# Kernel optimization log

Hardware: AMD Instinct MI355X
Metric: run time of the kernel (lower is better)

## Reference

```python
import jax, jax.numpy as jnp
import numpy as np

N_NODES = 100000
N_EDGES = 3200000
IN_DIM = 128
H1, F1 = 8, 8          # layer1: 8 heads x 8 feats -> concat 64
N_CLASSES = 40         # layer2: 1 head -> classes
NEG_SLOPE = 0.2        # GAT LeakyReLU slope


def setup_inputs() -> dict:
    key = jax.random.key(0)
    ks = jax.random.split(key, 8)
    x = jax.random.normal(ks[0], (N_NODES, IN_DIM), dtype=jnp.float32)
    adj = jax.random.randint(ks[1], (2, N_EDGES), 0, N_NODES, dtype=jnp.int64)
    s1 = 1.0 / np.sqrt(IN_DIM)
    s2 = 1.0 / np.sqrt(H1 * F1)
    W1 = jax.random.normal(ks[2], (IN_DIM, H1 * F1), dtype=jnp.float32) * s1
    a1_src = jax.random.normal(ks[3], (H1, F1), dtype=jnp.float32) * s2
    a1_dst = jax.random.normal(ks[4], (H1, F1), dtype=jnp.float32) * s2
    W2 = jax.random.normal(ks[5], (H1 * F1, N_CLASSES), dtype=jnp.float32) * s2
    a2_src = jax.random.normal(ks[6], (1, N_CLASSES), dtype=jnp.float32) * s2
    a2_dst = jax.random.normal(ks[7], (1, N_CLASSES), dtype=jnp.float32) * s2
    return {"input_matrix": x, "adjacency_coo_matrix": adj,
            "W1": W1, "a1_src": a1_src, "a1_dst": a1_dst,
            "W2": W2, "a2_src": a2_src, "a2_dst": a2_dst}


def gat_layer(x, src, dst, W, a_s, a_d, heads, fdim):
    n = x.shape[0]
    h = (x @ W).reshape(n, heads, fdim)                 # [N,H,F]
    e_src = jnp.sum(h * a_s, axis=-1)                   # [N,H]
    e_dst = jnp.sum(h * a_d, axis=-1)                   # [N,H]
    e = jax.nn.leaky_relu(e_src[src] + e_dst[dst], NEG_SLOPE)  # [E,H]
    m = jax.ops.segment_max(e, dst, num_segments=n)     # per-dst softmax max
    p = jnp.exp(e - m[dst])
    s = jax.ops.segment_sum(p, dst, num_segments=n)
    alpha = p / s[dst]                                  # [E,H]
    out = jax.ops.segment_sum(alpha[:, :, None] * h[src], dst, num_segments=n)
    return out                                          # [N,H,F]


def reference(input_matrix, adjacency_coo_matrix, W1, a1_src, a1_dst, W2, a2_src, a2_dst):
    n = input_matrix.shape[0]
    loops = jnp.arange(n, dtype=adjacency_coo_matrix.dtype)
    src = jnp.concatenate([adjacency_coo_matrix[0], loops])
    dst = jnp.concatenate([adjacency_coo_matrix[1], loops])
    x = gat_layer(input_matrix, src, dst, W1, a1_src, a1_dst, H1, F1)
    x = jax.nn.elu(x.reshape(n, H1 * F1))               # concat heads + ELU
    x = gat_layer(x, src, dst, W2, a2_src, a2_dst, 1, N_CLASSES)
    return jax.nn.log_softmax(x.reshape(n, N_CLASSES), axis=1)
```

## Files before the change

### kernel.cpp

```cpp
#include <hip/hip_runtime.h>
#include <hip/hip_fp16.h>
#include <math.h>

#define NN 100000
#define EE 3200000
#define ET (EE + NN)
#define BKW 128
#define NBK ((NN + BKW - 1) / BKW)
#define BCAP 5120
#define EPB 4096
#define NB_P1 ((EE + EPB - 1) / EPB)
#define NB_G 391

typedef float v2f __attribute__((ext_vector_type(2)));
typedef float v4f __attribute__((ext_vector_type(4)));
typedef _Float16 v8h __attribute__((ext_vector_type(8)));

__device__ __forceinline__ float lrelu(float v) { return fmaxf(v, 0.2f * v); }

__device__ __forceinline__ unsigned char to_fp8(float v) {
  return (unsigned char)(__builtin_amdgcn_cvt_pk_fp8_f32(v, v, 0, false) & 0xff);
}


__global__ __launch_bounds__(256) void k_p1(const int* __restrict__ srcs,
                                            const int* __restrict__ dsts,
                                            int* __restrict__ bcount,
                                            int* __restrict__ bbuf) {
  __shared__ int lcnt[NBK];
  __shared__ int lbase[NBK];
  int tid = threadIdx.x;
  for (int i = tid; i < NBK; i += 256) lcnt[i] = 0;
  __syncthreads();
  int e0 = blockIdx.x * EPB;
  int rank[16], bkt[16], pk[16];
#pragma unroll
  for (int i = 0; i < 16; ++i) {
    int e = e0 + tid + i * 256;
    bkt[i] = -1;
    if (e < EE) {
      int d = dsts[e];
      int s = srcs[e];
      int b = d >> 7;
      rank[i] = atomicAdd(&lcnt[b], 1);
      bkt[i] = b;
      pk[i] = (s << 7) | (d & 127);
    }
  }
  __syncthreads();
  for (int i = tid; i < NBK; i += 256) {
    int c = lcnt[i];
    lbase[i] = c ? atomicAdd(&bcount[i], c) : 0;
  }
  __syncthreads();
#pragma unroll
  for (int i = 0; i < 16; ++i) {
    if (bkt[i] >= 0) {
      bbuf[(size_t)bkt[i] * BCAP + lbase[bkt[i]] + rank[i]] = pk[i];
    }
  }
}

__global__ void k_bscan(const int* __restrict__ bcount, int* __restrict__ bbase) {
  __shared__ int s[1024];
  int t = threadIdx.x;
  int v = 0;
  if (t < NBK) v = bcount[t] + min(BKW, NN - (t << 7));
  s[t] = v;
  __syncthreads();
  for (int off = 1; off < 1024; off <<= 1) {
    int u = (t >= off) ? s[t - off] : 0;
    __syncthreads();
    s[t] += u;
    __syncthreads();
  }
  if (t < NBK) bbase[t] = s[t] - v;
}

__global__ __launch_bounds__(256) void k_p2(const int* __restrict__ bcount,
                                            const int* __restrict__ bbase,
                                            const int* __restrict__ bbuf,
                                            int* __restrict__ offsets,
                                            int* __restrict__ edge_src) {
  __shared__ int cnt[BKW];
  __shared__ int s1[BKW];
  __shared__ int cur[BKW];
  int b = blockIdx.x, tid = threadIdx.x;
  int d0 = b << 7;
  int width = min(BKW, NN - d0);
  int n = bcount[b];
  int base = bbase[b];
  const int* buf = bbuf + (size_t)b * BCAP;
  if (tid < BKW) cnt[tid] = (tid < width) ? 1 : 0;
  __syncthreads();
  for (int i = tid; i < n; i += 256) atomicAdd(&cnt[buf[i] & 127], 1);
  __syncthreads();
  if (tid < BKW) s1[tid] = cnt[tid];
  __syncthreads();
  for (int off = 1; off < BKW; off <<= 1) {
    int u = (tid < BKW && tid >= off) ? s1[tid - off] : 0;
    __syncthreads();
    if (tid < BKW) s1[tid] += u;
    __syncthreads();
  }
  if (tid < width) {
    int excl = s1[tid] - cnt[tid];
    offsets[d0 + tid] = base + excl;
    edge_src[base + excl] = d0 + tid;
    cur[tid] = excl + 1;
  }
  if (b == 0 && tid == 0) offsets[NN] = ET;
  __syncthreads();
  for (int i = tid; i < n; i += 256) {
    int p = buf[i];
    int pos = atomicAdd(&cur[p & 127], 1);
    edge_src[base + pos] = p >> 7;
  }
}


__global__ __launch_bounds__(256) void k_gemm1(
    const float* __restrict__ x, const float* __restrict__ W1,
    const float* __restrict__ a1d,
    unsigned char* __restrict__ P1, float* __restrict__ ed1) {
  __shared__ _Float16 Wb[16 * 64 * 8];
  int tid = threadIdx.x;
  for (int idx = tid; idx < 16 * 64; idx += 256) {
    int f = idx >> 6, l = idx & 63;
    int nt = f >> 2, kk = f & 3;
    int ql = l >> 4, cl = l & 15;
    int col = nt * 16 + cl;
    int k0 = kk * 32 + ql * 8;
    v8h tmp;
#pragma unroll
    for (int j = 0; j < 8; ++j) tmp[j] = (_Float16)W1[(k0 + j) * 64 + col];
    *reinterpret_cast<v8h*>(&Wb[idx * 8]) = tmp;
  }
  __syncthreads();
  int wv = tid >> 6, lane = tid & 63;
  int q = lane >> 4, c = lane & 15;
  v8h bf[16];
#pragma unroll
  for (int f = 0; f < 16; ++f)
    bf[f] = *reinterpret_cast<const v8h*>(&Wb[(f * 64 + lane) * 8]);
  float a1d_l[4];
#pragma unroll
  for (int nt = 0; nt < 4; ++nt) a1d_l[nt] = a1d[nt * 16 + c];
  for (int t = 0; t < 4; ++t) {
    int n0 = blockIdx.x * 256 + wv * 64 + t * 16;
    int row = n0 + c;
    row = (row < NN) ? row : (NN - 1);
    v4f acc[4] = {{0.f,0.f,0.f,0.f},{0.f,0.f,0.f,0.f},{0.f,0.f,0.f,0.f},{0.f,0.f,0.f,0.f}};
#pragma unroll
    for (int kk = 0; kk < 4; ++kk) {
      const float* xp = x + (size_t)row * 128 + kk * 32 + q * 8;
      float4 x0 = *reinterpret_cast<const float4*>(xp);
      float4 x1 = *reinterpret_cast<const float4*>(xp + 4);
      v8h af;
      af[0] = (_Float16)x0.x; af[1] = (_Float16)x0.y;
      af[2] = (_Float16)x0.z; af[3] = (_Float16)x0.w;
      af[4] = (_Float16)x1.x; af[5] = (_Float16)x1.y;
      af[6] = (_Float16)x1.z; af[7] = (_Float16)x1.w;
#pragma unroll
      for (int nt = 0; nt < 4; ++nt)
        acc[nt] = __builtin_amdgcn_mfma_f32_16x16x32_f16(af, bf[nt * 4 + kk], acc[nt], 0, 0, 0);
    }
#pragma unroll
    for (int nt = 0; nt < 4; ++nt) {
#pragma unroll
      for (int r = 0; r < 4; ++r) {
        float val = acc[nt][r];
        float vd = val * a1d_l[nt];
        vd += __shfl_xor(vd, 1); vd += __shfl_xor(vd, 2); vd += __shfl_xor(vd, 4);
        int node = n0 + q * 4 + r;
        if (node < NN) {
          P1[((size_t)node << 6) + nt * 16 + c] = to_fp8(val);
          if ((c & 7) == 0) ed1[node * 8 + 2 * nt + (c >> 3)] = vd;
        }
      }
    }
  }
}


__global__ __launch_bounds__(256) void k_agg1(
    const int* __restrict__ offsets, const int* __restrict__ edge_src,
    const unsigned char* __restrict__ P1, const float* __restrict__ a1s,
    const float* __restrict__ ed1, __half* __restrict__ x2) {
  int wv = threadIdx.x >> 6, lane = threadIdx.x & 63;
  int g = lane >> 3, p = lane & 7;
  int dst = blockIdx.x * 32 + wv * 8 + g;
  float edv = ed1[dst * 8 + p];
  float4 as0 = *reinterpret_cast<const float4*>(a1s + p * 8);
  float4 as1 = *reinterpret_cast<const float4*>(a1s + p * 8 + 4);
  int beg = offsets[dst], end = offsets[dst + 1];
  int deg = end - beg;
  int md = deg;
#pragma unroll
  for (int o = 8; o < 64; o <<= 1) md = max(md, __shfl_xor(md, o, 64));
  float l = 0.f;
  float a[8] = {0.f, 0.f, 0.f, 0.f, 0.f, 0.f, 0.f, 0.f};
  for (int t = 0; t < md; t += 8) {
    int src[8]; uint2 raw[8];
#pragma unroll
    for (int i = 0; i < 8; ++i) {
      int idx = t + i;
      int ci = beg + ((idx < deg) ? idx : (deg - 1));
      src[i] = edge_src[ci];
    }
#pragma unroll
    for (int i = 0; i < 8; ++i)
      raw[i] = *reinterpret_cast<const uint2*>(P1 + ((size_t)src[i] << 6) + (p << 3));
#pragma unroll
    for (int i = 0; i < 8; ++i) {
      v2f f01 = __builtin_amdgcn_cvt_pk_f32_fp8(raw[i].x, false);
      v2f f23 = __builtin_amdgcn_cvt_pk_f32_fp8(raw[i].x, true);
      v2f f45 = __builtin_amdgcn_cvt_pk_f32_fp8(raw[i].y, false);
      v2f f67 = __builtin_amdgcn_cvt_pk_f32_fp8(raw[i].y, true);
      float es = f01.x * as0.x + f01.y * as0.y + f23.x * as0.z + f23.y * as0.w
               + f45.x * as1.x + f45.y * as1.y + f67.x * as1.z + f67.y * as1.w;
      float e = lrelu(es + edv);
      float pr = (t + i < deg) ? __expf(e) : 0.f;
      l += pr;
      a[0] += pr * f01.x; a[1] += pr * f01.y;
      a[2] += pr * f23.x; a[3] += pr * f23.y;
      a[4] += pr * f45.x; a[5] += pr * f45.y;
      a[6] += pr * f67.x; a[7] += pr * f67.y;
    }
  }
  float rl = 1.f / l;
  union { __half h[8]; uint4 u; } pk;
#pragma unroll
  for (int i = 0; i < 8; ++i) {
    float v = a[i] * rl;
    v = (v > 0.f) ? v : (__expf(v) - 1.f);
    pk.h[i] = __float2half(v);
  }
  *reinterpret_cast<uint4*>(x2 + ((size_t)dst << 6) + (p << 3)) = pk.u;
}


__global__ __launch_bounds__(256) void k_gemm2(
    const __half* __restrict__ x2, const float* __restrict__ W2,
    const float* __restrict__ a2s, const float* __restrict__ a2d,
    unsigned char* __restrict__ P2, float* __restrict__ ed2) {
  __shared__ _Float16 Wb[6 * 64 * 8];
  int tid = threadIdx.x;
  for (int idx = tid; idx < 6 * 64; idx += 256) {
    int f = idx >> 6, l = idx & 63;
    int nt = f >> 1, kk = f & 1;
    int ql = l >> 4, cl = l & 15;
    int col = nt * 16 + cl;
    int k0 = kk * 32 + ql * 8;
    v8h tmp;
#pragma unroll
    for (int j = 0; j < 8; ++j)
      tmp[j] = (col < 40) ? (_Float16)W2[(k0 + j) * 40 + col] : (_Float16)0.f;
    *reinterpret_cast<v8h*>(&Wb[idx * 8]) = tmp;
  }
  __syncthreads();
  int wv = tid >> 6, lane = tid & 63;
  int q = lane >> 4, c = lane & 15;
  v8h bf[6];
#pragma unroll
  for (int f = 0; f < 6; ++f)
    bf[f] = *reinterpret_cast<const v8h*>(&Wb[(f * 64 + lane) * 8]);
  float a2s_l[3], a2d_l[3];
#pragma unroll
  for (int nt = 0; nt < 3; ++nt) {
    int n = nt * 16 + c;
    a2s_l[nt] = (n < 40) ? a2s[n] : 0.f;
    a2d_l[nt] = (n < 40) ? a2d[n] : 0.f;
  }
  for (int t = 0; t < 4; ++t) {
    int n0 = blockIdx.x * 256 + wv * 64 + t * 16;
    int row = n0 + c;
    row = (row < NN) ? row : (NN - 1);
    v4f acc[3] = {{0.f,0.f,0.f,0.f},{0.f,0.f,0.f,0.f},{0.f,0.f,0.f,0.f}};
#pragma unroll
    for (int kk = 0; kk < 2; ++kk) {
      v8h af = *reinterpret_cast<const v8h*>(x2 + (size_t)row * 64 + kk * 32 + q * 8);
#pragma unroll
      for (int nt = 0; nt < 3; ++nt)
        acc[nt] = __builtin_amdgcn_mfma_f32_16x16x32_f16(af, bf[nt * 2 + kk], acc[nt], 0, 0, 0);
    }
#pragma unroll
    for (int r = 0; r < 4; ++r) {
      float v0 = acc[0][r], v1 = acc[1][r], v2 = acc[2][r];
      float s = v0 * a2s_l[0] + v1 * a2s_l[1] + v2 * a2s_l[2];
      float d = v0 * a2d_l[0] + v1 * a2d_l[1] + v2 * a2d_l[2];
      s += __shfl_xor(s, 1); s += __shfl_xor(s, 2); s += __shfl_xor(s, 4); s += __shfl_xor(s, 8);
      d += __shfl_xor(d, 1); d += __shfl_xor(d, 2); d += __shfl_xor(d, 4); d += __shfl_xor(d, 8);
      int node = n0 + q * 4 + r;
      if (node < NN) {
        unsigned char* rec = P2 + ((size_t)node << 6);
        if (c < 8) rec[32 + c] = to_fp8(v2);
        rec[c]      = to_fp8(v0);
        rec[16 + c] = to_fp8(v1);
        if (c == 0) {
          *reinterpret_cast<__half*>(rec + 40) = __float2half(s);
          ed2[node] = d;
        }
      }
    }
  }
}


__global__ __launch_bounds__(256) void k_agg2(
    const int* __restrict__ offsets, const int* __restrict__ edge_src,
    const unsigned char* __restrict__ P2, const float* __restrict__ ed2,
    float* __restrict__ out) {
  int wv = threadIdx.x >> 6, lane = threadIdx.x & 63;
  int g = lane >> 4, p = lane & 15;
  bool act = p < 10;
  int cp = act ? p : 0;
  int dst = blockIdx.x * 16 + wv * 4 + g;
  float edv = ed2[dst];
  int beg = offsets[dst], end = offsets[dst + 1];
  int deg = end - beg;
  int md = deg;
#pragma unroll
  for (int o = 16; o < 64; o <<= 1) md = max(md, __shfl_xor(md, o, 64));
  int gbase = lane & 48;
  int me = p & 7;
  float l = 0.f;
  float a[4] = {0.f, 0.f, 0.f, 0.f};
  for (int t = 0; t < md; t += 8) {
    int src[8]; unsigned raw[8];
#pragma unroll
    for (int i = 0; i < 8; ++i) {
      int ix = t + i;
      int ci = beg + ((ix < deg) ? ix : (deg - 1));
      src[i] = edge_src[ci];
    }
    float myes = __half2float(*reinterpret_cast<const __half*>(
        P2 + ((size_t)src[me] << 6) + 40));
    float mye = lrelu(myes + edv);
    float mypr = (t + me < deg) ? __expf(mye) : 0.f;
#pragma unroll
    for (int i = 0; i < 8; ++i)
      raw[i] = *reinterpret_cast<const unsigned*>(P2 + ((size_t)src[i] << 6) + (cp << 2));
#pragma unroll
    for (int i = 0; i < 8; ++i) {
      float pr = __shfl(mypr, gbase | i, 64);
      v2f f01 = __builtin_amdgcn_cvt_pk_f32_fp8(raw[i], false);
      v2f f23 = __builtin_amdgcn_cvt_pk_f32_fp8(raw[i], true);
      l += pr;
      a[0] += pr * f01.x; a[1] += pr * f01.y;
      a[2] += pr * f23.x; a[3] += pr * f23.y;
    }
  }
  float rl = 1.f / l;
  float v0 = a[0] * rl, v1 = a[1] * rl, v2 = a[2] * rl, v3 = a[3] * rl;
  float red = act ? fmaxf(fmaxf(v0, v1), fmaxf(v2, v3)) : -INFINITY;
#pragma unroll
  for (int o = 1; o < 16; o <<= 1) red = fmaxf(red, __shfl_xor(red, o, 64));
  float se = act ? (__expf(v0 - red) + __expf(v1 - red) + __expf(v2 - red) + __expf(v3 - red)) : 0.f;
#pragma unroll
  for (int o = 1; o < 16; o <<= 1) se += __shfl_xor(se, o, 64);
  float ls = red + __logf(se);
  if (act) {
    float4 o4 = make_float4(v0 - ls, v1 - ls, v2 - ls, v3 - ls);
    *reinterpret_cast<float4*>(out + (size_t)dst * 40 + (p << 2)) = o4;
  }
}


extern "C" void kernel_launch(void* const* d_in, const int* in_sizes, int n_in,
                              void* d_out, int out_size, void* d_ws, size_t ws_size,
                              hipStream_t stream) {
  const float* x   = (const float*)d_in[0];
  const int*   adj = (const int*)d_in[1];
  const float* W1  = (const float*)d_in[2];
  const float* a1s = (const float*)d_in[3];
  const float* a1d = (const float*)d_in[4];
  const float* W2  = (const float*)d_in[5];
  const float* a2s = (const float*)d_in[6];
  const float* a2d = (const float*)d_in[7];
  float* out = (float*)d_out;

  const int* srcs = adj;
  const int* dsts = adj + EE;

  char* w = (char*)d_ws;
  size_t off = 0;
  auto alloc = [&](size_t bytes) -> void* {
    void* p = w + off;
    off = (off + bytes + 255) & ~(size_t)255;
    return p;
  };
  int* offsets      = (int*)alloc((size_t)(NN + 1) * 4);
  int* edge_src     = (int*)alloc((size_t)ET * 4);
  int* bcount       = (int*)alloc((size_t)NBK * 4);
  int* bbase        = (int*)alloc((size_t)NBK * 4);
  unsigned char* P1 = (unsigned char*)alloc((size_t)NN * 64);
  float* ed1        = (float*)alloc((size_t)NN * 8 * 4);
  __half* x2        = (__half*)alloc((size_t)NN * 64 * 2);
  int* bbuf         = (int*)alloc((size_t)NBK * BCAP * 4);
  unsigned char* P2 = P1;
  float* ed2 = ed1;

  hipMemsetAsync(bcount, 0, (size_t)NBK * 4, stream);
  k_p1<<<NB_P1, 256, 0, stream>>>(srcs, dsts, bcount, bbuf);
  k_bscan<<<1, 1024, 0, stream>>>(bcount, bbase);
  k_p2<<<NBK, 256, 0, stream>>>(bcount, bbase, bbuf, offsets, edge_src);

  k_gemm1<<<NB_G, 256, 0, stream>>>(x, W1, a1d, P1, ed1);
  k_agg1<<<NN / 32, 256, 0, stream>>>(offsets, edge_src, P1, a1s, ed1, x2);
  k_gemm2<<<NB_G, 256, 0, stream>>>(x2, W2, a2s, a2d, P2, ed2);
  k_agg2<<<NN / 16, 256, 0, stream>>>(offsets, edge_src, P2, ed2, out);
}
```

Baseline: 307.3 us.

## Merge edge bucketing with layer-1 GEMM and fold bucket scan into p2

Runs the edge-bucketing pass and the layer-1 GEMM as one horizontally fused launch, with blocks split by index and shared memory reused between the two roles. The separate single-block scan kernel is removed; each p2 block now computes its own base offset by reducing the bucket counts before it. This cuts two launches and the serial scan step, letting independent work share the GPU. In exchange each p2 block repeats a reduction of up to ~782 counts, which is redundant work.

```diff
diff --git a/kernel.cpp b/kernel.cpp
--- a/kernel.cpp
+++ b/kernel.cpp
@@ -23,108 +23,50 @@
 }
 
 
-__global__ __launch_bounds__(256) void k_p1(const int* __restrict__ srcs,
-                                            const int* __restrict__ dsts,
-                                            int* __restrict__ bcount,
-                                            int* __restrict__ bbuf) {
-  __shared__ int lcnt[NBK];
-  __shared__ int lbase[NBK];
-  int tid = threadIdx.x;
-  for (int i = tid; i < NBK; i += 256) lcnt[i] = 0;
-  __syncthreads();
-  int e0 = blockIdx.x * EPB;
-  int rank[16], bkt[16], pk[16];
-#pragma unroll
-  for (int i = 0; i < 16; ++i) {
-    int e = e0 + tid + i * 256;
-    bkt[i] = -1;
-    if (e < EE) {
-      int d = dsts[e];
-      int s = srcs[e];
-      int b = d >> 7;
-      rank[i] = atomicAdd(&lcnt[b], 1);
-      bkt[i] = b;
-      pk[i] = (s << 7) | (d & 127);
-    }
-  }
-  __syncthreads();
-  for (int i = tid; i < NBK; i += 256) {
-    int c = lcnt[i];
-    lbase[i] = c ? atomicAdd(&bcount[i], c) : 0;
-  }
-  __syncthreads();
-#pragma unroll
-  for (int i = 0; i < 16; ++i) {
-    if (bkt[i] >= 0) {
-      bbuf[(size_t)bkt[i] * BCAP + lbase[bkt[i]] + rank[i]] = pk[i];
-    }
-  }
-}
-
-__global__ void k_bscan(const int* __restrict__ bcount, int* __restrict__ bbase) {
-  __shared__ int s[1024];
-  int t = threadIdx.x;
-  int v = 0;
-  if (t < NBK) v = bcount[t] + min(BKW, NN - (t << 7));
-  s[t] = v;
-  __syncthreads();
-  for (int off = 1; off < 1024; off <<= 1) {
-    int u = (t >= off) ? s[t - off] : 0;
-    __syncthreads();
-    s[t] += u;
-    __syncthreads();
-  }
-  if (t < NBK) bbase[t] = s[t] - v;
-}
-
-__global__ __launch_bounds__(256) void k_p2(const int* __restrict__ bcount,
-                                            const int* __restrict__ bbase,
-                                            const int* __restrict__ bbuf,
-                                            int* __restrict__ offsets,
-                                            int* __restrict__ edge_src) {
-  __shared__ int cnt[BKW];
-  __shared__ int s1[BKW];
-  __shared__ int cur[BKW];
-  int b = blockIdx.x, tid = threadIdx.x;
-  int d0 = b << 7;
-  int width = min(BKW, NN - d0);
-  int n = bcount[b];
-  int base = bbase[b];
-  const int* buf = bbuf + (size_t)b * BCAP;
-  if (tid < BKW) cnt[tid] = (tid < width) ? 1 : 0;
-  __syncthreads();
-  for (int i = tid; i < n; i += 256) atomicAdd(&cnt[buf[i] & 127], 1);
-  __syncthreads();
-  if (tid < BKW) s1[tid] = cnt[tid];
-  __syncthreads();
-  for (int off = 1; off < BKW; off <<= 1) {
-    int u = (tid < BKW && tid >= off) ? s1[tid - off] : 0;
-    __syncthreads();
-    if (tid < BKW) s1[tid] += u;
-    __syncthreads();
-  }
-  if (tid < width) {
-    int excl = s1[tid] - cnt[tid];
-    offsets[d0 + tid] = base + excl;
-    edge_src[base + excl] = d0 + tid;
-    cur[tid] = excl + 1;
-  }
-  if (b == 0 && tid == 0) offsets[NN] = ET;
-  __syncthreads();
-  for (int i = tid; i < n; i += 256) {
-    int p = buf[i];
-    int pos = atomicAdd(&cur[p & 127], 1);
-    edge_src[base + pos] = p >> 7;
-  }
-}
-
-
-__global__ __launch_bounds__(256) void k_gemm1(
+__global__ __launch_bounds__(256) void k_p1g1(
+    const int* __restrict__ srcs, const int* __restrict__ dsts,
+    int* __restrict__ bcount, int* __restrict__ bbuf,
     const float* __restrict__ x, const float* __restrict__ W1,
     const float* __restrict__ a1d,
     unsigned char* __restrict__ P1, float* __restrict__ ed1) {
-  __shared__ _Float16 Wb[16 * 64 * 8];
+  __shared__ char smem[16 * 64 * 8 * 2];
   int tid = threadIdx.x;
+  if (blockIdx.x < NB_P1) {
+    int* lcnt  = (int*)smem;
+    int* lbase = lcnt + NBK;
+    for (int i = tid; i < NBK; i += 256) lcnt[i] = 0;
+    __syncthreads();
+    int e0 = blockIdx.x * EPB;
+    int rank[16], bkt[16], pk[16];
+#pragma unroll
+    for (int i = 0; i < 16; ++i) {
+      int e = e0 + tid + i * 256;
+      bkt[i] = -1;
+      if (e < EE) {
+        int d = dsts[e];
+        int s = srcs[e];
+        int b = d >> 7;
+        rank[i] = atomicAdd(&lcnt[b], 1);
+        bkt[i] = b;
+        pk[i] = (s << 7) | (d & 127);
+      }
+    }
+    __syncthreads();
+    for (int i = tid; i < NBK; i += 256) {
+      int c = lcnt[i];
+      lbase[i] = c ? atomicAdd(&bcount[i], c) : 0;
+    }
+    __syncthreads();
+#pragma unroll
+    for (int i = 0; i < 16; ++i) {
+      if (bkt[i] >= 0) {
+        bbuf[(size_t)bkt[i] * BCAP + lbase[bkt[i]] + rank[i]] = pk[i];
+      }
+    }
+    return;
+  }
+  _Float16* Wb = (_Float16*)smem;
+  int gbid = blockIdx.x - NB_P1;
   for (int idx = tid; idx < 16 * 64; idx += 256) {
     int f = idx >> 6, l = idx & 63;
     int nt = f >> 2, kk = f & 3;
@@ -147,7 +89,7 @@
 #pragma unroll
   for (int nt = 0; nt < 4; ++nt) a1d_l[nt] = a1d[nt * 16 + c];
   for (int t = 0; t < 4; ++t) {
-    int n0 = blockIdx.x * 256 + wv * 64 + t * 16;
+    int n0 = gbid * 256 + wv * 64 + t * 16;
     int row = n0 + c;
     row = (row < NN) ? row : (NN - 1);
     v4f acc[4] = {{0.f,0.f,0.f,0.f},{0.f,0.f,0.f,0.f},{0.f,0.f,0.f,0.f},{0.f,0.f,0.f,0.f}};
@@ -179,6 +121,57 @@
         }
       }
     }
+  }
+}
+
+
+__global__ __launch_bounds__(256) void k_p2(const int* __restrict__ bcount,
+                                            const int* __restrict__ bbuf,
+                                            int* __restrict__ offsets,
+                                            int* __restrict__ edge_src) {
+  __shared__ int cnt[BKW];
+  __shared__ int s1[BKW];
+  __shared__ int cur[BKW];
+  __shared__ int red[256];
+  int b = blockIdx.x, tid = threadIdx.x;
+  int partial = 0;
+  for (int j = tid; j < b; j += 256)
+    partial += bcount[j] + min(BKW, NN - (j << 7));
+  red[tid] = partial;
+  __syncthreads();
+  for (int off = 128; off >= 1; off >>= 1) {
+    if (tid < off) red[tid] += red[tid + off];
+    __syncthreads();
+  }
+  int base = red[0];
+  int d0 = b << 7;
+  int width = min(BKW, NN - d0);
+  int n = bcount[b];
+  const int* buf = bbuf + (size_t)b * BCAP;
+  if (tid < BKW) cnt[tid] = (tid < width) ? 1 : 0;
+  __syncthreads();
+  for (int i = tid; i < n; i += 256) atomicAdd(&cnt[buf[i] & 127], 1);
+  __syncthreads();
+  if (tid < BKW) s1[tid] = cnt[tid];
+  __syncthreads();
+  for (int off = 1; off < BKW; off <<= 1) {
+    int u = (tid < BKW && tid >= off) ? s1[tid - off] : 0;
+    __syncthreads();
+    if (tid < BKW) s1[tid] += u;
+    __syncthreads();
+  }
+  if (tid < width) {
+    int excl = s1[tid] - cnt[tid];
+    offsets[d0 + tid] = base + excl;
+    edge_src[base + excl] = d0 + tid;
+    cur[tid] = excl + 1;
+  }
+  if (b == 0 && tid == 0) offsets[NN] = ET;
+  __syncthreads();
+  for (int i = tid; i < n; i += 256) {
+    int p = buf[i];
+    int pos = atomicAdd(&cur[p & 127], 1);
+    edge_src[base + pos] = p >> 7;
   }
 }
 
@@ -393,7 +386,6 @@
   int* offsets      = (int*)alloc((size_t)(NN + 1) * 4);
   int* edge_src     = (int*)alloc((size_t)ET * 4);
   int* bcount       = (int*)alloc((size_t)NBK * 4);
-  int* bbase        = (int*)alloc((size_t)NBK * 4);
   unsigned char* P1 = (unsigned char*)alloc((size_t)NN * 64);
   float* ed1        = (float*)alloc((size_t)NN * 8 * 4);
   __half* x2        = (__half*)alloc((size_t)NN * 64 * 2);
@@ -402,11 +394,10 @@
   float* ed2 = ed1;
 
   hipMemsetAsync(bcount, 0, (size_t)NBK * 4, stream);
-  k_p1<<<NB_P1, 256, 0, stream>>>(srcs, dsts, bcount, bbuf);
-  k_bscan<<<1, 1024, 0, stream>>>(bcount, bbase);
-  k_p2<<<NBK, 256, 0, stream>>>(bcount, bbase, bbuf, offsets, edge_src);
-
-  k_gemm1<<<NB_G, 256, 0, stream>>>(x, W1, a1d, P1, ed1);
+  k_p1g1<<<NB_P1 + NB_G, 256, 0, stream>>>(srcs, dsts, bcount, bbuf,
+                                           x, W1, a1d, P1, ed1);
+  k_p2<<<NBK, 256, 0, stream>>>(bcount, bbuf, offsets, edge_src);
+
   k_agg1<<<NN / 32, 256, 0, stream>>>(offsets, edge_src, P1, a1s, ed1, x2);
   k_gemm2<<<NB_G, 256, 0, stream>>>(x2, W2, a2s, a2d, P2, ed2);
   k_agg2<<<NN / 16, 256, 0, stream>>>(offsets, edge_src, P2, ed2, out);
```

Measured after the change: 299.6 us. 1.03x faster.
